# Optimization experiments

Measured on AMD Instinct MI355X. Metric: run time of the kernel, lower is better.

The kernel has to match this reference:

```python
import jax, jax.numpy as jnp
import numpy as np

B, S, V, E, U, L = 32, 256, 32000, 512, 512, 2

def setup_inputs() -> dict:
    key = jax.random.key(0)
    ks = jax.random.split(key, 16)
    def p(k, shape, scale):
        return jax.random.normal(k, shape, dtype=jnp.float32) * scale
    inp = {
        "x": jax.random.randint(ks[0], (B, S), 0, V),
        "state": jnp.zeros((2 * L, B, U), jnp.float32),
        "emb_table": p(ks[1], (V, E), 0.05),
    }
    names = ["fk0", "frk0", "fb0", "fk1", "frk1", "fb1",
             "bk0", "brk0", "bb0", "bk1", "brk1", "bb1"]
    i = 2
    for n in names:
        if n.endswith("b0") or n.endswith("b1"):
            inp[n] = jnp.zeros((2, 3 * U), jnp.float32)
        else:
            inp[n] = p(ks[i], (512, 3 * U), 1.0 / np.sqrt(512))
        i += 1
    return inp

def gru_step(h, xt, k, rk, b):
    # TF2 GRUCell, reset_after=True
    mx = xt @ k + b[0]
    mi = h @ rk + b[1]
    xz, xr, xh = jnp.split(mx, 3, axis=-1)
    iz, ir, ih = jnp.split(mi, 3, axis=-1)
    z = jax.nn.sigmoid(xz + iz)
    r = jax.nn.sigmoid(xr + ir)
    hh = jnp.tanh(xh + r * ih)
    return z * h + (1.0 - z) * hh

def run_rnn(emb_s, mask_s, h0s, params):
    # emb_s: [S,B,E], mask_s: [S,B], h0s: tuple of L x [B,U]
    def step(carry, inp):
        hs, prev = carry
        xt, mt = inp
        m = mt[:, None]
        new_hs = []
        a = xt
        for h, (k, rk, b) in zip(hs, params):
            hn = gru_step(h, a, k, rk, b)
            hn = jnp.where(m, hn, h)  # masked steps carry state
            new_hs.append(hn)
            a = hn
        out = jnp.where(m, a, prev)  # masked steps repeat prev output
        return (tuple(new_hs), out), out
    init = (tuple(h0s), jnp.zeros((emb_s.shape[1], U), emb_s.dtype))
    (hs_f, _), ys = jax.lax.scan(step, init, (emb_s, mask_s))
    return ys, hs_f

def reference(x, state, emb_table,
              fk0, frk0, fb0, fk1, frk1, fb1,
              bk0, brk0, bb0, bk1, brk1, bb1):
    emb = emb_table[x]                      # [B,S,E]
    mask = (x != 0)                         # mask_zero=True
    emb_s = jnp.swapaxes(emb, 0, 1)         # [S,B,E]
    mask_s = jnp.swapaxes(mask, 0, 1)       # [S,B]
    fw_params = [(fk0, frk0, fb0), (fk1, frk1, fb1)]
    bw_params = [(bk0, brk0, bb0), (bk1, brk1, bb1)]
    ys_f, hs_f = run_rnn(emb_s, mask_s, (state[0], state[1]), fw_params)
    ys_b, hs_b = run_rnn(emb_s[::-1], mask_s[::-1], (state[2], state[3]), bw_params)
    ys_b = ys_b[::-1]
    y = jnp.concatenate([ys_f, ys_b], axis=-1)   # [S,B,2U]
    y = jnp.swapaxes(y, 0, 1)                    # [B,S,2U]
    states = jnp.stack(list(hs_f) + list(hs_b), axis=0)  # [2L,B,U]
    return y, states
```

## Files before the change

### kernel.cpp

```cpp
#include <hip/hip_runtime.h>
#include <hip/hip_bf16.h>

#define S_LEN 256
#define NB 32
#define UDIM 512
#define WGS 32

typedef __attribute__((ext_vector_type(8))) short bf16x8;
typedef __attribute__((ext_vector_type(4))) float f32x4;
typedef __attribute__((ext_vector_type(4))) unsigned u32x4;

struct WPtrs { const float* p[8]; };
struct BPtrs { const float* p[4]; };

#define SLAB(c, slot) ((((size_t)(c) * 257 + (slot)) * 32) << 10)

__device__ __forceinline__ unsigned short f2bf(float f) {
  union { float f; unsigned u; } v; v.f = f;
  unsigned r = v.u + 0x7fffu + ((v.u >> 16) & 1u);
  return (unsigned short)(r >> 16);
}

__device__ __forceinline__ int ld_flag(const int* p) {
  int v;
  asm volatile("global_load_dword %0, %1, off sc0 sc1\n\ts_waitcnt vmcnt(0)"
               : "=&v"(v) : "v"(p) : "memory");
  return v;
}
__device__ __forceinline__ void st_u32c(void* p, unsigned v) {
  asm volatile("global_store_dword %0, %1, off sc0 sc1" :: "v"(p), "v"(v) : "memory");
}
__device__ __forceinline__ void st_flag(int* p, int v) {
  asm volatile("global_store_dword %0, %1, off sc0 sc1" :: "v"(p), "v"(v) : "memory");
}

__device__ __forceinline__ bool ld_slab16(const char* b0, const char* b1,
                                          const char* b2, const char* b3,
                                          bf16x8* afr0, bf16x8* afr1) {
  u32x4 q0,q1,q2,q3,q4,q5,q6,q7,q8,q9,q10,q11,q12,q13,q14,q15;
  asm volatile(
    "global_load_dwordx4 %0, %16, off sc0 sc1\n\t"
    "global_load_dwordx4 %1, %16, off offset:512 sc0 sc1\n\t"
    "global_load_dwordx4 %2, %16, off offset:2048 sc0 sc1\n\t"
    "global_load_dwordx4 %3, %16, off offset:2560 sc0 sc1\n\t"
    "global_load_dwordx4 %4, %17, off sc0 sc1\n\t"
    "global_load_dwordx4 %5, %17, off offset:512 sc0 sc1\n\t"
    "global_load_dwordx4 %6, %17, off offset:2048 sc0 sc1\n\t"
    "global_load_dwordx4 %7, %17, off offset:2560 sc0 sc1\n\t"
    "global_load_dwordx4 %8, %18, off sc0 sc1\n\t"
    "global_load_dwordx4 %9, %18, off offset:512 sc0 sc1\n\t"
    "global_load_dwordx4 %10, %18, off offset:2048 sc0 sc1\n\t"
    "global_load_dwordx4 %11, %18, off offset:2560 sc0 sc1\n\t"
    "global_load_dwordx4 %12, %19, off sc0 sc1\n\t"
    "global_load_dwordx4 %13, %19, off offset:512 sc0 sc1\n\t"
    "global_load_dwordx4 %14, %19, off offset:2048 sc0 sc1\n\t"
    "global_load_dwordx4 %15, %19, off offset:2560 sc0 sc1\n\t"
    "s_waitcnt vmcnt(0)"
    : "=&v"(q0),"=&v"(q1),"=&v"(q2),"=&v"(q3),"=&v"(q4),"=&v"(q5),"=&v"(q6),"=&v"(q7),
      "=&v"(q8),"=&v"(q9),"=&v"(q10),"=&v"(q11),"=&v"(q12),"=&v"(q13),"=&v"(q14),"=&v"(q15)
    : "v"(b0), "v"(b1), "v"(b2), "v"(b3)
    : "memory");
  const unsigned S = 0xFFFFFFFFu;
  bool bad = false;
#define CK(q) bad |= (q[0]==S)|(q[1]==S)|(q[2]==S)|(q[3]==S)
  CK(q0);CK(q1);CK(q2);CK(q3);CK(q4);CK(q5);CK(q6);CK(q7);
  CK(q8);CK(q9);CK(q10);CK(q11);CK(q12);CK(q13);CK(q14);CK(q15);
#undef CK
  union U { u32x4 u; bf16x8 b; } cv;
  cv.u=q0;  afr0[0]=cv.b; cv.u=q1;  afr1[0]=cv.b; cv.u=q2;  afr0[1]=cv.b; cv.u=q3;  afr1[1]=cv.b;
  cv.u=q4;  afr0[2]=cv.b; cv.u=q5;  afr1[2]=cv.b; cv.u=q6;  afr0[3]=cv.b; cv.u=q7;  afr1[3]=cv.b;
  cv.u=q8;  afr0[4]=cv.b; cv.u=q9;  afr1[4]=cv.b; cv.u=q10; afr0[5]=cv.b; cv.u=q11; afr1[5]=cv.b;
  cv.u=q12; afr0[6]=cv.b; cv.u=q13; afr1[6]=cv.b; cv.u=q14; afr0[7]=cv.b; cv.u=q15; afr1[7]=cv.b;
  return !bad;
}

__global__ void k_embed(const int* __restrict__ x, const float* __restrict__ tab,
                        unsigned short* __restrict__ emb, int* __restrict__ mask) {
  int t = blockIdx.x, b = blockIdx.y;
  int tok = x[b * S_LEN + t];
  if (threadIdx.x == 0) mask[t * NB + b] = (tok != 0);
  const float4* src = (const float4*)(tab + (size_t)tok * UDIM);
  ushort4* dst = (ushort4*)(emb + ((size_t)t * NB + b) * UDIM);
  int i = threadIdx.x;
  float4 v = src[i];
  ushort4 o;
  o.x = f2bf(v.x); o.y = f2bf(v.y); o.z = f2bf(v.z); o.w = f2bf(v.w);
  dst[i] = o;
}

__global__ void k_wprep(WPtrs wp, unsigned short* __restrict__ wsW) {
  int bid = blockIdx.x;
  int kt = bid & 31; bid >>= 5;
  int g  = bid % 3;  bid /= 3;
  int wg = bid & 31; bid >>= 5;
  int slab = bid;
  const float* src = wp.p[slab];
  int tid = threadIdx.x;
  int r = tid >> 4, cc = tid & 15;
  __shared__ float ldsT[16][17];
  ldsT[cc][r] = src[(size_t)(kt * 16 + r) * 1536 + g * 512 + wg * 16 + cc];
  __syncthreads();
  size_t off = ((size_t)slab * WGS + wg) * (48 * 512) + (size_t)(g * 16 + r) * 512 + kt * 16 + cc;
  wsW[off] = f2bf(ldsT[r][cc]);
}

__global__ __launch_bounds__(256, 1) void k_rnn(
    const unsigned short* __restrict__ wsW, const unsigned short* __restrict__ emb,
    unsigned short* __restrict__ hist, const int* __restrict__ mask,
    int* __restrict__ flags, const float* __restrict__ state,
    BPtrs bp, float* __restrict__ out) {
  __shared__ short sW[2 * 48 * 512];
  __shared__ float sAcc[2][2][2][32][48];
  __shared__ float sBias[2][48];
  __shared__ unsigned char sMask[S_LEN][NB];

  int tid = threadIdx.x;
  int bid = blockIdx.x;
  int xcd = bid & 7;
  int c = xcd >> 1;
  int w = ((bid >> 3) << 1) | (xcd & 1);
  int layer = c & 1;
  bool back = (c >= 2);
  int lane = tid & 63;
  int wave = tid >> 6;
  int mat = wave & 1;
  int kh = wave >> 1;

  int cb = tid >> 3;
  int cj = (tid & 7) << 1;
  float hreg0, hreg1, preg0 = 0.f, preg1 = 0.f;

  char* histc = (char*)hist;

  {
    const size_t slabSz = 48 * 512;
    for (int ch = tid; ch < 2 * 48 * 64; ch += 256) {
      int m = ch / (48 * 64);
      int rem = ch % (48 * 64);
      int nl = rem >> 6;
      int k16 = rem & 63;
      const unsigned short* sp =
          wsW + ((size_t)((c * 2 + m) * WGS) + w) * slabSz + (size_t)nl * 512 + k16 * 8;
      bf16x8 val = *(const bf16x8*)sp;
      int byte = m * 49152 + nl * 1024 + ((k16 * 16) ^ ((nl & 7) << 4));
      *(bf16x8*)((char*)sW + byte) = val;
    }
    const float* bptr = bp.p[c];
    for (int i = tid; i < 96; i += 256) {
      int m = i / 48, nl = i % 48;
      int col = (nl / 16) * 512 + w * 16 + (nl & 15);
      sBias[m][nl] = bptr[m * 1536 + col];
    }
    for (int i = tid; i < S_LEN * NB; i += 256)
      sMask[i >> 5][i & 31] = (unsigned char)(mask[i] != 0);
    int col = w * 16 + cj;
    hreg0 = state[((size_t)c * NB + cb) * UDIM + col];
    hreg1 = state[((size_t)c * NB + cb) * UDIM + col + 1];
    unsigned pk = (unsigned)f2bf(hreg0) | ((unsigned)f2bf(hreg1) << 16);
    st_u32c(histc + SLAB(c, 0) + ((size_t)w << 10) + cb * 32 + cj * 2, pk);
  }
  __syncthreads();
  if (tid == 0) st_flag(&flags[(c * 257) * 32 + w], 1);

  int r15 = lane & 15, quad = lane >> 4;
  int lbase = ((kh * 16 + (quad >> 1)) << 10) + ((quad & 1) << 4) + r15 * 32;
  int abase = r15 * UDIM + kh * 256 + quad * 8;
  int matbase = mat * 49152;

  for (int t = 0; t < S_LEN; ++t) {
    int par = t & 1;
    int treal = back ? (S_LEN - 1 - t) : t;

    bf16x8 afr0[8], afr1[8];
    if (mat == 0 && layer == 0) {
      const short* a16 = (const short*)(emb + (size_t)treal * NB * UDIM);
#pragma unroll
      for (int kc = 0; kc < 8; ++kc) {
        afr0[kc] = *(const bf16x8*)(a16 + abase + kc * 32);
        afr1[kc] = *(const bf16x8*)(a16 + abase + 16 * UDIM + kc * 32);
      }
    } else {
      const int* fl;
      const char* sb;
      int ownIdx = -1;
      if (mat == 0) {
        sb = histc + SLAB(c - 1, t + 1);
        fl = flags + ((c - 1) * 257 + (t + 1)) * 32;
      } else {
        sb = histc + SLAB(c, t);
        fl = flags + (c * 257 + t) * 32;
        ownIdx = w;
      }
      const int* fp = fl + (lane & 31);
      bool sub = ((lane & 31) == ownIdx);
      int v = sub ? 1 : ld_flag(fp);
      while (!__all(v != 0)) v = sub ? 1 : ld_flag(fp);
      const char* b0 = sb + lbase;
      bool ok = ld_slab16(b0, b0 + 4096, b0 + 8192, b0 + 12288, afr0, afr1);
      while (!__all(ok))
        ok = ld_slab16(b0, b0 + 4096, b0 + 8192, b0 + 12288, afr0, afr1);
    }

    f32x4 acc[2][3];
#pragma unroll
    for (int a = 0; a < 2; a++)
#pragma unroll
      for (int g = 0; g < 3; g++) acc[a][g] = (f32x4){0.f, 0.f, 0.f, 0.f};
#pragma unroll
    for (int kc = 0; kc < 8; ++kc) {
#pragma unroll
      for (int g = 0; g < 3; ++g) {
        int nl = g * 16 + r15;
        int koff = kh * 512 + kc * 64 + quad * 16;
        int byte = matbase + nl * 1024 + (koff ^ ((nl & 7) << 4));
        bf16x8 bw = *(const bf16x8*)((const char*)sW + byte);
        acc[0][g] = __builtin_amdgcn_mfma_f32_16x16x32_bf16(afr0[kc], bw, acc[0][g], 0, 0, 0);
        acc[1][g] = __builtin_amdgcn_mfma_f32_16x16x32_bf16(afr1[kc], bw, acc[1][g], 0, 0, 0);
      }
    }
#pragma unroll
    for (int mt = 0; mt < 2; ++mt)
#pragma unroll
      for (int g = 0; g < 3; ++g)
#pragma unroll
        for (int rr = 0; rr < 4; ++rr)
          sAcc[par][kh][mat][mt * 16 + quad * 4 + rr][g * 16 + r15] = acc[mt][g][rr];
    __syncthreads();

    float hn0, hn1;
    bool mk;
    {
      int b = cb, j0 = cj;
      mk = sMask[treal][b] != 0;
#pragma unroll
      for (int u = 0; u < 2; ++u) {
        int j = j0 + u;
        float az = sAcc[par][0][0][b][j]      + sAcc[par][1][0][b][j]      + sBias[0][j];
        float ar = sAcc[par][0][0][b][16 + j] + sAcc[par][1][0][b][16 + j] + sBias[0][16 + j];
        float ah = sAcc[par][0][0][b][32 + j] + sAcc[par][1][0][b][32 + j] + sBias[0][32 + j];
        float iz = sAcc[par][0][1][b][j]      + sAcc[par][1][1][b][j]      + sBias[1][j];
        float ir = sAcc[par][0][1][b][16 + j] + sAcc[par][1][1][b][16 + j] + sBias[1][16 + j];
        float ih = sAcc[par][0][1][b][32 + j] + sAcc[par][1][1][b][32 + j] + sBias[1][32 + j];
        float z = 1.f / (1.f + __expf(-(az + iz)));
        float r = 1.f / (1.f + __expf(-(ar + ir)));
        float pre = ah + r * ih;
        pre = fminf(fmaxf(pre, -30.f), 30.f);
        float e2 = __expf(2.f * pre);
        float hh = (e2 - 1.f) / (e2 + 1.f);
        float hold = (u == 0) ? hreg0 : hreg1;
        float hv = z * hold + (1.f - z) * hh;
        hv = mk ? hv : hold;
        if (u == 0) hn0 = hv; else hn1 = hv;
      }
      hreg0 = hn0; hreg1 = hn1;
      unsigned pk = (unsigned)f2bf(hn0) | ((unsigned)f2bf(hn1) << 16);
      st_u32c(histc + SLAB(c, t + 1) + ((size_t)w << 10) + cb * 32 + cj * 2, pk);
    }
    __builtin_amdgcn_s_barrier();
    if (tid == 0) st_flag(&flags[(c * 257 + (t + 1)) * 32 + w], 1);

    if (layer == 1) {
      float o0 = mk ? hn0 : preg0;
      float o1 = mk ? hn1 : preg1;
      preg0 = o0; preg1 = o1;
      *(float2*)(out + ((size_t)cb * S_LEN + treal) * 1024 + (back ? 512 : 0) + w * 16 + cj) =
          make_float2(o0, o1);
    }
    if (t == S_LEN - 1) {
      *(float2*)(out + (size_t)NB * S_LEN * 1024 + ((size_t)c * NB + cb) * UDIM + w * 16 + cj) =
          make_float2(hn0, hn1);
    }
  }
}

extern "C" void kernel_launch(void* const* d_in, const int* in_sizes, int n_in,
                              void* d_out, int out_size, void* d_ws, size_t ws_size,
                              hipStream_t stream) {
  const int* x = (const int*)d_in[0];
  const float* state = (const float*)d_in[1];
  const float* tab = (const float*)d_in[2];
  WPtrs wp;
  wp.p[0] = (const float*)d_in[3];
  wp.p[1] = (const float*)d_in[4];
  wp.p[2] = (const float*)d_in[6];
  wp.p[3] = (const float*)d_in[7];
  wp.p[4] = (const float*)d_in[9];
  wp.p[5] = (const float*)d_in[10];
  wp.p[6] = (const float*)d_in[12];
  wp.p[7] = (const float*)d_in[13];
  BPtrs bp;
  bp.p[0] = (const float*)d_in[5];
  bp.p[1] = (const float*)d_in[8];
  bp.p[2] = (const float*)d_in[11];
  bp.p[3] = (const float*)d_in[14];
  float* out = (float*)d_out;

  char* ws = (char*)d_ws;
  size_t off = 0;
  unsigned short* wsW = (unsigned short*)(ws + off); off += (size_t)8 * 32 * 48 * 512 * 2;
  unsigned short* embp = (unsigned short*)(ws + off); off += (size_t)S_LEN * NB * UDIM * 2;
  unsigned short* hist = (unsigned short*)(ws + off);
  size_t histBytes = (size_t)4 * 257 * 32 * 1024;      off += histBytes;
  int* maskp = (int*)(ws + off); off += (size_t)S_LEN * NB * 4;
  int* flags = (int*)(ws + off);
  size_t flagBytes = (size_t)4 * 257 * 32 * 4;         off += flagBytes;

  hipMemsetAsync(hist, 0xFF, histBytes, stream);
  hipMemsetAsync(flags, 0, flagBytes, stream);
  k_embed<<<dim3(S_LEN, NB), 128, 0, stream>>>(x, tab, embp, maskp);
  k_wprep<<<8 * 32 * 3 * 32, 256, 0, stream>>>(wp, wsW);
  k_rnn<<<128, 256, 0, stream>>>(wsW, embp, hist, maskp, flags, state, bp, out);
}
```

Baseline: 994.6 us.

## Replace per-step flag handshakes with polling on sentinel-filled hidden-state data

Drops the separate flag array and its per-step barrier-plus-flag store. Consumers now spin on one word of each producer's hidden-state slab until it differs from the 0xFFFFFFFF fill value, then load the full slab, which still retries until no sentinel remains. This removes a barrier and a flag round-trip from the recurrent critical path, and the flag memset. It relies on the last-written word appearing only when the rest of the slab is ready, and the existing retry loop on the slab load is the safety net if that ordering does not hold.

Measured after the change: 977.1 us, median of 2. No clear change (-1.8%).

```diff
diff --git a/kernel.cpp b/kernel.cpp
--- a/kernel.cpp
+++ b/kernel.cpp
@@ -21,16 +21,13 @@
   return (unsigned short)(r >> 16);
 }
 
-__device__ __forceinline__ int ld_flag(const int* p) {
-  int v;
+__device__ __forceinline__ unsigned ld_word_coh(const char* p) {
+  unsigned v;
   asm volatile("global_load_dword %0, %1, off sc0 sc1\n\ts_waitcnt vmcnt(0)"
                : "=&v"(v) : "v"(p) : "memory");
   return v;
 }
 __device__ __forceinline__ void st_u32c(void* p, unsigned v) {
-  asm volatile("global_store_dword %0, %1, off sc0 sc1" :: "v"(p), "v"(v) : "memory");
-}
-__device__ __forceinline__ void st_flag(int* p, int v) {
   asm volatile("global_store_dword %0, %1, off sc0 sc1" :: "v"(p), "v"(v) : "memory");
 }
 
@@ -107,8 +104,7 @@
 __global__ __launch_bounds__(256, 1) void k_rnn(
     const unsigned short* __restrict__ wsW, const unsigned short* __restrict__ emb,
     unsigned short* __restrict__ hist, const int* __restrict__ mask,
-    int* __restrict__ flags, const float* __restrict__ state,
-    BPtrs bp, float* __restrict__ out) {
+    const float* __restrict__ state, BPtrs bp, float* __restrict__ out) {
   __shared__ short sW[2 * 48 * 512];
   __shared__ float sAcc[2][2][2][32][48];
   __shared__ float sBias[2][48];
@@ -160,10 +156,11 @@
     st_u32c(histc + SLAB(c, 0) + ((size_t)w << 10) + cb * 32 + cj * 2, pk);
   }
   __syncthreads();
-  if (tid == 0) st_flag(&flags[(c * 257) * 32 + w], 1);
 
   int r15 = lane & 15, quad = lane >> 4;
   int lbase = ((kh * 16 + (quad >> 1)) << 10) + ((quad & 1) << 4) + r15 * 32;
+  int hoff = ((kh * 16 + (lane & 15)) << 10) + ((((lane >> 4) << 1) + 1) << 7) + 124;
+  bool ownHint = (kh * 16 + (lane & 15)) == w;
   int abase = r15 * UDIM + kh * 256 + quad * 8;
   int matbase = mat * 49152;
 
@@ -180,21 +177,15 @@
         afr1[kc] = *(const bf16x8*)(a16 + abase + 16 * UDIM + kc * 32);
       }
     } else {
-      const int* fl;
       const char* sb;
-      int ownIdx = -1;
-      if (mat == 0) {
-        sb = histc + SLAB(c - 1, t + 1);
-        fl = flags + ((c - 1) * 257 + (t + 1)) * 32;
-      } else {
-        sb = histc + SLAB(c, t);
-        fl = flags + (c * 257 + t) * 32;
-        ownIdx = w;
-      }
-      const int* fp = fl + (lane & 31);
-      bool sub = ((lane & 31) == ownIdx);
-      int v = sub ? 1 : ld_flag(fp);
-      while (!__all(v != 0)) v = sub ? 1 : ld_flag(fp);
+      bool skipOwn;
+      if (mat == 0) { sb = histc + SLAB(c - 1, t + 1); skipOwn = false; }
+      else          { sb = histc + SLAB(c, t);          skipOwn = true; }
+      const char* hp = sb + hoff;
+      bool own = skipOwn && ownHint;
+      unsigned hv = own ? 0u : ld_word_coh(hp);
+      while (!__all(own || hv != 0xFFFFFFFFu))
+        hv = own ? 0u : ld_word_coh(hp);
       const char* b0 = sb + lbase;
       bool ok = ld_slab16(b0, b0 + 4096, b0 + 8192, b0 + 12288, afr0, afr1);
       while (!__all(ok))
@@ -256,8 +247,6 @@
       unsigned pk = (unsigned)f2bf(hn0) | ((unsigned)f2bf(hn1) << 16);
       st_u32c(histc + SLAB(c, t + 1) + ((size_t)w << 10) + cb * 32 + cj * 2, pk);
     }
-    __builtin_amdgcn_s_barrier();
-    if (tid == 0) st_flag(&flags[(c * 257 + (t + 1)) * 32 + w], 1);
 
     if (layer == 1) {
       float o0 = mk ? hn0 : preg0;
@@ -302,12 +291,9 @@
   unsigned short* hist = (unsigned short*)(ws + off);
   size_t histBytes = (size_t)4 * 257 * 32 * 1024;      off += histBytes;
   int* maskp = (int*)(ws + off); off += (size_t)S_LEN * NB * 4;
-  int* flags = (int*)(ws + off);
-  size_t flagBytes = (size_t)4 * 257 * 32 * 4;         off += flagBytes;
 
   hipMemsetAsync(hist, 0xFF, histBytes, stream);
-  hipMemsetAsync(flags, 0, flagBytes, stream);
   k_embed<<<dim3(S_LEN, NB), 128, 0, stream>>>(x, tab, embp, maskp);
   k_wprep<<<8 * 32 * 3 * 32, 256, 0, stream>>>(wp, wsW);
-  k_rnn<<<128, 256, 0, stream>>>(wsW, embp, hist, maskp, flags, state, bp, out);
-}
+  k_rnn<<<128, 256, 0, stream>>>(wsW, embp, hist, maskp, state, bp, out);
+}
```
